# Performance work log

Hardware: AMD Instinct MI355X
Metric: run time of the kernel (lower is better)

Reference implementation:

```python
import jax, jax.numpy as jnp
import numpy as np

N = 100_000   # nodes
E = 1_600_000 # edges
V = 100_000   # vocab
G = 256       # graphs in batch
D = 64        # emb/hidden dim


def setup_inputs() -> dict:
    key = jax.random.key(0)
    ks = jax.random.split(key, 12)
    x_tokens = jax.random.randint(ks[0], (N, 1), 0, V)
    edge_index = jax.random.randint(ks[1], (2, E), 0, N)
    batch = jnp.sort(jax.random.randint(ks[2], (N,), 0, G))
    s = 0.02
    return {
        "x_tokens": x_tokens,
        "edge_index": edge_index,
        "batch": batch,
        "emb_table": jax.random.normal(ks[3], (V, D), jnp.float32) * s,
        "W0": jax.random.normal(ks[4], (D, D), jnp.float32) * s,
        "b0": jnp.zeros((D,), jnp.float32),
        "W1": jax.random.normal(ks[5], (D, D), jnp.float32) * s,
        "b1": jnp.zeros((D,), jnp.float32),
        "W2": jax.random.normal(ks[6], (D, D), jnp.float32) * s,
        "b2": jnp.zeros((D,), jnp.float32),
        "Wc1": jax.random.normal(ks[7], (2 * D, D), jnp.float32) * s,
        "bc1": jnp.zeros((D,), jnp.float32),
        "Wc2": jax.random.normal(ks[8], (D, 2), jnp.float32) * s,
        "bc2": jnp.zeros((2,), jnp.float32),
    }


def _gcn_norm(edge_index, n_nodes):
    # add self loops, compute symmetric normalization coefficients
    loop = jnp.arange(n_nodes, dtype=edge_index.dtype)
    src = jnp.concatenate([edge_index[0], loop])
    dst = jnp.concatenate([edge_index[1], loop])
    deg = jax.ops.segment_sum(jnp.ones_like(dst, jnp.float32), dst, num_segments=n_nodes)
    dinv = jnp.where(deg > 0, deg ** -0.5, 0.0)
    norm = dinv[src] * dinv[dst]  # [E+N]
    return src, dst, norm


def _gcn_conv(x, W, b, src, dst, norm, n_nodes):
    x = x @ W                                   # [N, D]
    msg = x[src] * norm[:, None]                # gather + scale, [E+N, D]
    out = jax.ops.segment_sum(msg, dst, num_segments=n_nodes)
    return out + b


def reference(x_tokens, edge_index, batch, emb_table, W0, b0, W1, b1, W2, b2, Wc1, bc1, Wc2, bc2):
    n = x_tokens.shape[0]
    src, dst, norm = _gcn_norm(edge_index, n)
    x = emb_table[x_tokens[:, 0]]               # [N, D]
    for W, b in ((W0, b0), (W1, b1), (W2, b2)):
        x = jax.nn.relu(_gcn_conv(x, W, b, src, dst, norm, n))
    # dual pooling over graph ids
    cnt = jax.ops.segment_sum(jnp.ones((n,), x.dtype), batch, num_segments=G)
    h_sum = jax.ops.segment_sum(x, batch, num_segments=G)
    h_mean = h_sum / jnp.maximum(cnt, 1.0)[:, None]
    h_max = jax.ops.segment_max(x, batch, num_segments=G)
    h_max = jnp.where(jnp.isfinite(h_max), h_max, 0.0)
    h = jnp.concatenate([h_mean, h_max], axis=-1)   # [G, 2D]
    logits = jax.nn.relu(h @ Wc1 + bc1) @ Wc2 + bc2  # [G, 2]
    return logits
```

## Files before the change

kernel.cpp:

```cpp
#include <hip/hip_runtime.h>
#include <hip/hip_fp16.h>
#include <math.h>


#define BKT_LOG 9
#define BKT (1 << BKT_LOG)
#define CHUNK 4096

typedef _Float16 h2 __attribute__((ext_vector_type(2)));
typedef _Float16 f16x8 __attribute__((ext_vector_type(8)));
typedef float f32x4 __attribute__((ext_vector_type(4)));

union HU { unsigned u; h2 h; };
__device__ inline h2 h2bits(unsigned u) { HU x; x.u = u; return x.h; }

#if __has_builtin(__builtin_amdgcn_fdot2)
#define FDOT2(a, b, c) __builtin_amdgcn_fdot2((a), (b), (c), false)
#else
__device__ inline float FDOT2(h2 a, h2 b, float c) {
  return (float)a.x * (float)b.x + (float)a.y * (float)b.y + c;
}
#endif

#define MASK_X 0x00003C00u
#define MASK_Y 0x3C000000u

__device__ inline void acc8c(const uint4& v, float* acc) {
  const unsigned* w = (const unsigned*)&v;
#pragma unroll
  for (int k = 0; k < 4; k++) {
    h2 hv = h2bits(w[k]);
    acc[2 * k]     = FDOT2(hv, h2bits(MASK_X), acc[2 * k]);
    acc[2 * k + 1] = FDOT2(hv, h2bits(MASK_Y), acc[2 * k + 1]);
  }
}

__global__ __launch_bounds__(256) void k_wcvt(const float* __restrict__ W0,
                                              const float* __restrict__ W1,
                                              const float* __restrict__ W2,
                                              _Float16* __restrict__ Wf,
                                              int* __restrict__ chist,
                                              float* __restrict__ hz, int hzn) {
  if (blockIdx.x < 3) {
    const float* W = (blockIdx.x == 0) ? W0 : (blockIdx.x == 1) ? W1 : W2;
    _Float16* out = Wf + blockIdx.x * 4096;
    for (int i = threadIdx.x; i < 4096; i += 256) {
      int c = i >> 10, s = (i >> 9) & 1, l = (i >> 3) & 63, j = i & 7;
      int k = 32 * s + 8 * (l >> 4) + j;
      int ncol = 16 * c + (l & 15);
      out[i] = (_Float16)W[k * 64 + ncol];
    }
  } else if (blockIdx.x == 3) {
    chist[threadIdx.x] = 0;
  } else {
    for (int i = threadIdx.x; i < hzn; i += 256) hz[i] = 0.f;
  }
}

__global__ __launch_bounds__(256) void k_chist(const int* __restrict__ dst,
                                               int* __restrict__ chist, int E, int B) {
  __shared__ int h[256];
  h[threadIdx.x] = 0;
  __syncthreads();
  for (long e = (long)blockIdx.x * blockDim.x + threadIdx.x; e < E;
       e += (long)gridDim.x * blockDim.x)
    atomicAdd(&h[dst[e] >> BKT_LOG], 1);
  __syncthreads();
  if (threadIdx.x < B && h[threadIdx.x]) atomicAdd(&chist[threadIdx.x], h[threadIdx.x]);
}

__global__ __launch_bounds__(256) void k_cscan(const int* __restrict__ chist,
                                               int* __restrict__ cbase,
                                               int* __restrict__ gcur, int E, int B) {
  __shared__ int s[256];
  int v = (threadIdx.x < B) ? chist[threadIdx.x] : 0;
  s[threadIdx.x] = v;
  __syncthreads();
  for (int d = 1; d < 256; d <<= 1) {
    int t = (threadIdx.x >= (unsigned)d) ? s[threadIdx.x - d] : 0;
    __syncthreads();
    s[threadIdx.x] += t;
    __syncthreads();
  }
  if (threadIdx.x < B) {
    int ex = s[threadIdx.x] - v;
    cbase[threadIdx.x] = ex;
    gcur[threadIdx.x] = ex;
  }
  if (threadIdx.x == B) cbase[B] = E;
}

__global__ __launch_bounds__(256) void k_part(const int* __restrict__ src,
                                              const int* __restrict__ dst,
                                              int* __restrict__ gcur,
                                              int* __restrict__ ebuf, int E, int B) {
  __shared__ int sA[CHUNK];
  __shared__ int dA[CHUNK];
  __shared__ int h[256], base[256];
  int tid = threadIdx.x;
  long c0 = (long)blockIdx.x * CHUNK;
  int m = (int)min((long)CHUNK, (long)E - c0);
  h[tid] = 0;
  __syncthreads();
  for (int i = tid; i < m; i += 256) {
    int s = src[c0 + i];
    int d = dst[c0 + i];
    sA[i] = s;
    dA[i] = d;
    atomicAdd(&h[d >> BKT_LOG], 1);
  }
  __syncthreads();
  if (tid < B && h[tid]) base[tid] = atomicAdd(&gcur[tid], h[tid]);
  __syncthreads();
  h[tid] = 0;
  __syncthreads();
  for (int i = tid; i < m; i += 256) {
    int s = sA[i], d = dA[i];
    int k = d >> BKT_LOG;
    int p = base[k] + atomicAdd(&h[k], 1);
    ebuf[p] = ((d & (BKT - 1)) << 17) | s;
  }
}

__global__ __launch_bounds__(512) void k_bplace(const int* __restrict__ ebuf,
                                                const int* __restrict__ cbase,
                                                int* __restrict__ off,
                                                int* __restrict__ csrc,
                                                float* __restrict__ dinv,
                                                int N, int E) {
  __shared__ int s[512];
  __shared__ int cur[512];
  int b = blockIdx.x, tid = threadIdx.x;
  int n0 = b << BKT_LOG;
  int nn = min(BKT, N - n0);
  int e0 = cbase[b], e1 = cbase[b + 1];
  s[tid] = 0;
  __syncthreads();
  for (int e = e0 + tid; e < e1; e += 512) atomicAdd(&s[ebuf[e] >> 17], 1);
  __syncthreads();
  int deg = s[tid];
  for (int d = 1; d < 512; d <<= 1) {
    int t = (tid >= d) ? s[tid - d] : 0;
    __syncthreads();
    s[tid] += t;
    __syncthreads();
  }
  int excl = s[tid] - deg;
  if (tid < nn) {
    off[n0 + tid] = e0 + excl;
    dinv[n0 + tid] = 1.0f / sqrtf((float)(1 + deg));
  }
  cur[tid] = excl;
  __syncthreads();
  for (int e = e0 + tid; e < e1; e += 512) {
    int p = ebuf[e];
    int pos = e0 + atomicAdd(&cur[p >> 17], 1);
    csrc[pos] = p & 0x1FFFF;
  }
  if (b == 0 && tid == 0) off[N] = E;
}

template <bool EMB>
__global__ __launch_bounds__(256) void k_mfmamm(const _Float16* __restrict__ y,
                                                const int* __restrict__ tok,
                                                const float* __restrict__ emb,
                                                const _Float16* __restrict__ Wf,
                                                const float* __restrict__ dinv,
                                                float scale,
                                                _Float16* __restrict__ xh,
                                                int n, int npad) {
  __shared__ _Float16 lds[4 * 16 * 72];
  int w = threadIdx.x >> 6, l = threadIdx.x & 63;
  int m = l & 15, q = l >> 4;
  int rbase = blockIdx.x * 64 + w * 16;

  f16x8 a0, a1;
  if (EMB) {
    int node = min(rbase + m, n - 1);
    const float* er = emb + (size_t)tok[node] * 64;
    float4 v0 = *(const float4*)(er + q * 8);
    float4 v1 = *(const float4*)(er + q * 8 + 4);
    float4 v2 = *(const float4*)(er + 32 + q * 8);
    float4 v3 = *(const float4*)(er + 32 + q * 8 + 4);
    a0[0] = (_Float16)v0.x; a0[1] = (_Float16)v0.y; a0[2] = (_Float16)v0.z; a0[3] = (_Float16)v0.w;
    a0[4] = (_Float16)v1.x; a0[5] = (_Float16)v1.y; a0[6] = (_Float16)v1.z; a0[7] = (_Float16)v1.w;
    a1[0] = (_Float16)v2.x; a1[1] = (_Float16)v2.y; a1[2] = (_Float16)v2.z; a1[3] = (_Float16)v2.w;
    a1[4] = (_Float16)v3.x; a1[5] = (_Float16)v3.y; a1[6] = (_Float16)v3.z; a1[7] = (_Float16)v3.w;
  } else {
    int node = rbase + m;
    a0 = *(const f16x8*)(y + ((size_t)(q >> 1) * npad + node) * 16 + (q & 1) * 8);
    a1 = *(const f16x8*)(y + ((size_t)((q >> 1) + 2) * npad + node) * 16 + (q & 1) * 8);
  }
  float4 d4 = *(const float4*)(dinv + rbase + q * 4);

  const f16x8* wf = (const f16x8*)Wf + l;
  f32x4 acc[4];
#pragma unroll
  for (int c = 0; c < 4; c++) {
    f32x4 z = {0.f, 0.f, 0.f, 0.f};
    z = __builtin_amdgcn_mfma_f32_16x16x32_f16(a0, wf[(c * 2 + 0) * 64], z, 0, 0, 0);
    z = __builtin_amdgcn_mfma_f32_16x16x32_f16(a1, wf[(c * 2 + 1) * 64], z, 0, 0, 0);
    acc[c] = z;
  }

  const float ds[4] = {d4.x * scale, d4.y * scale, d4.z * scale, d4.w * scale};
  _Float16* ldw = lds + w * 16 * 72;
#pragma unroll
  for (int c = 0; c < 4; c++)
#pragma unroll
    for (int r = 0; r < 4; r++)
      ldw[(q * 4 + r) * 72 + c * 16 + m] = (_Float16)(acc[c][r] * ds[r]);
  __syncthreads();

  int row2 = l & 15, c2 = l >> 4;
  int node = rbase + row2;
  if (node < n) {
    const uint4* s4 = (const uint4*)(ldw + row2 * 72 + c2 * 16);
    uint4 v0 = s4[0], v1 = s4[1];
    uint4* dst = (uint4*)(xh + ((size_t)c2 * npad + node) * 16);
    dst[0] = v0;
    dst[1] = v1;
  }
}

__global__ __launch_bounds__(256) void k_aggregate(const int* __restrict__ off,
                                                   const int* __restrict__ csrc,
                                                   const float* __restrict__ dinv,
                                                   const _Float16* __restrict__ xh,
                                                   const float* __restrict__ bias,
                                                   _Float16* __restrict__ outp,
                                                   int n, int npad) {
  int c = blockIdx.x & 3;
  int lane = threadIdx.x & 63;
  int n4 = lane >> 4, g = (lane >> 1) & 7, o = lane & 1;
  int t = (blockIdx.x >> 2) * 16 + (threadIdx.x >> 6) * 4 + n4;
  bool valid = t < n;
  int tc = valid ? t : n - 1;
  int e0 = off[tc], e1 = off[tc + 1];
  if (!valid) e1 = e0;
  const uint4* x4 = (const uint4*)xh + (size_t)c * npad * 2;

  float acc[8];
#pragma unroll
  for (int k = 0; k < 8; k++) acc[k] = 0.f;
  if (g == 0) acc8c(x4[(size_t)tc * 2 + o], acc);

  int it = e0 + g;
  int s = (it < e1) ? csrc[it] : 0;
  while (it < e1) {
    int itn = it + 8;
    int sn = (itn < e1) ? csrc[itn] : 0;
    uint4 v = x4[(size_t)s * 2 + o];
    acc8c(v, acc);
    s = sn;
    it = itn;
  }

#pragma unroll
  for (int mm = 2; mm <= 8; mm <<= 1) {
#pragma unroll
    for (int k = 0; k < 8; k++) acc[k] += __shfl_xor(acc[k], mm);
  }

  if (valid && g == 0) {
    float sc = dinv[t] * (1.0f / 256.0f);
    int f0 = c * 16 + o * 8;
    float4 bb0 = *(const float4*)(bias + f0);
    float4 bb1 = *(const float4*)(bias + f0 + 4);
    const float bs[8] = {bb0.x, bb0.y, bb0.z, bb0.w, bb1.x, bb1.y, bb1.z, bb1.w};
    _Float16 hh[8];
#pragma unroll
    for (int k = 0; k < 8; k++)
      hh[k] = (_Float16)(fmaxf(acc[k] * sc + bs[k], 0.f) * 4096.f);
    *(uint4*)(outp + ((size_t)c * npad + t) * 16 + o * 8) = *(const uint4*)hh;
  }
}

__global__ __launch_bounds__(256) void k_pool(const _Float16* __restrict__ x,
                                              const int* __restrict__ batch,
                                              float* __restrict__ hsum,
                                              float* __restrict__ hmax,
                                              int* __restrict__ cntg,
                                              int n, int npad) {
  int wid = (blockIdx.x * blockDim.x + threadIdx.x) >> 6;
  int lane = threadIdx.x & 63;
  int i0 = wid * 64;
  if (i0 >= n) return;
  int i1 = min(i0 + 64, n);
  size_t sb = (size_t)(lane >> 4) * npad * 16 + (lane & 15);
  int batch_l = (i0 + lane < n) ? batch[i0 + lane] : 0;
  float gsum = 0.f, gmax = 0.f;
  int cur = __shfl(batch_l, 0);
  int c = 0;
  for (int i = i0; i < i1; i++) {
    int g = __shfl(batch_l, i - i0);
    if (g != cur) {
      atomicAdd(&hsum[cur * 64 + lane], gsum);
      atomicMax((int*)&hmax[cur * 64 + lane], __float_as_int(gmax));
      if (lane == 0) atomicAdd(&cntg[cur], c);
      gsum = 0.f; gmax = 0.f; c = 0; cur = g;
    }
    float v = (float)x[sb + (size_t)i * 16];
    gsum += v;
    gmax = fmaxf(gmax, v);
    c++;
  }
  atomicAdd(&hsum[cur * 64 + lane], gsum);
  atomicMax((int*)&hmax[cur * 64 + lane], __float_as_int(gmax));
  if (lane == 0) atomicAdd(&cntg[cur], c);
}

__global__ __launch_bounds__(64) void k_cls(const float* __restrict__ hsum,
                                            const float* __restrict__ hmax,
                                            const int* __restrict__ cnt,
                                            const float* __restrict__ Wc1,
                                            const float* __restrict__ bc1,
                                            const float* __restrict__ Wc2,
                                            const float* __restrict__ bc2,
                                            float* __restrict__ out) {
  __shared__ float h[128];
  __shared__ float hid[64];
  int g = blockIdx.x, j = threadIdx.x;
  int c = cnt[g];
  float cf = (float)(c > 0 ? c : 1);
  h[j] = hsum[g * 64 + j] / cf * (1.0f / 4096.0f);
  h[64 + j] = hmax[g * 64 + j] * (1.0f / 4096.0f);
  __syncthreads();
  float acc = bc1[j];
  for (int k = 0; k < 128; k++) acc += h[k] * Wc1[k * 64 + j];
  hid[j] = fmaxf(acc, 0.f);
  __syncthreads();
  if (j < 2) {
    float a = bc2[j];
    for (int k = 0; k < 64; k++) a += hid[k] * Wc2[k * 2 + j];
    out[g * 2 + j] = a;
  }
}

extern "C" void kernel_launch(void* const* d_in, const int* in_sizes, int n_in,
                              void* d_out, int out_size, void* d_ws, size_t ws_size,
                              hipStream_t stream) {
  const int N = in_sizes[0];
  const int E = in_sizes[1] / 2;
  const int G = out_size / 2;
  const int B = (N + BKT - 1) >> BKT_LOG;
  const int Npad = (N + 63) & ~63;

  const int* tok   = (const int*)d_in[0];
  const int* ei    = (const int*)d_in[1];
  const int* batch = (const int*)d_in[2];
  const float* emb = (const float*)d_in[3];
  const float* W0 = (const float*)d_in[4];  const float* b0 = (const float*)d_in[5];
  const float* W1 = (const float*)d_in[6];  const float* b1 = (const float*)d_in[7];
  const float* W2 = (const float*)d_in[8];  const float* b2 = (const float*)d_in[9];
  const float* Wc1 = (const float*)d_in[10]; const float* bc1 = (const float*)d_in[11];
  const float* Wc2 = (const float*)d_in[12]; const float* bc2 = (const float*)d_in[13];
  const int* srcp = ei;
  const int* dstp = ei + E;

  int* off    = (int*)d_ws;
  int* csrc   = off + N + 2;
  float* dinv = (float*)(csrc + E);
  int* chist  = (int*)(dinv + Npad);
  int* cbase  = chist + 256;
  int* gcur   = cbase + 256;
  _Float16* Wf = (_Float16*)(gcur + 256);
  _Float16* xh = Wf + 3 * 4096;
  _Float16* y  = xh + (size_t)Npad * 64;
  int* ebuf   = (int*)(y + (size_t)Npad * 64);
  float* hsum = (float*)(ebuf + E);
  float* hmax = hsum + (size_t)G * 64;
  int*   cntg = (int*)(hmax + (size_t)G * 64);

  auto cdiv = [](long a, long b) { return (int)((a + b - 1) / b); };
  const int aggBlocks = 4 * cdiv(N, 16);

  k_wcvt<<<5, 256, 0, stream>>>(W0, W1, W2, Wf, chist, hsum, G * 129);

  k_chist<<<cdiv(E, CHUNK), 256, 0, stream>>>(dstp, chist, E, B);
  k_cscan<<<1, 256, 0, stream>>>(chist, cbase, gcur, E, B);
  k_part<<<cdiv(E, CHUNK), 256, 0, stream>>>(srcp, dstp, gcur, ebuf, E, B);
  k_bplace<<<B, 512, 0, stream>>>(ebuf, cbase, off, csrc, dinv, N, E);

  k_mfmamm<true><<<cdiv(N, 64), 256, 0, stream>>>(nullptr, tok, emb, Wf, dinv, 256.f, xh, N, Npad);
  k_aggregate<<<aggBlocks, 256, 0, stream>>>(off, csrc, dinv, xh, b0, y, N, Npad);

  k_mfmamm<false><<<cdiv(N, 64), 256, 0, stream>>>(y, nullptr, nullptr, Wf + 4096, dinv, 1.f / 16.f, xh, N, Npad);
  k_aggregate<<<aggBlocks, 256, 0, stream>>>(off, csrc, dinv, xh, b1, y, N, Npad);

  k_mfmamm<false><<<cdiv(N, 64), 256, 0, stream>>>(y, nullptr, nullptr, Wf + 8192, dinv, 1.f / 16.f, xh, N, Npad);
  k_aggregate<<<aggBlocks, 256, 0, stream>>>(off, csrc, dinv, xh, b2, y, N, Npad);

  k_pool<<<cdiv(N, 256), 256, 0, stream>>>(y, batch, hsum, hmax, cntg, N, Npad);

  k_cls<<<G, 64, 0, stream>>>(hsum, hmax, cntg, Wc1, bc1, Wc2, bc2, (float*)d_out);
}
```

Measured before the change: 371.8 us.

## Fold bucket scan into histogram via last-block pattern; unroll aggregate gather by two

Removes the separate single-block scan launch by having the last block of the histogram kernel (detected with an atomic counter and threadfence) perform the prefix scan. Separately, the aggregation edge loop now issues two neighbor row loads per iteration with index prefetch, raising memory-level parallelism. This saves one launch and gap at the cost of an extra counter reset and more registers in the aggregation kernel.

```diff
diff --git a/kernel.cpp b/kernel.cpp
--- a/kernel.cpp
+++ b/kernel.cpp
@@ -40,6 +40,7 @@
                                               const float* __restrict__ W2,
                                               _Float16* __restrict__ Wf,
                                               int* __restrict__ chist,
+                                              int* __restrict__ done,
                                               float* __restrict__ hz, int hzn) {
   if (blockIdx.x < 3) {
     const float* W = (blockIdx.x == 0) ? W0 : (blockIdx.x == 1) ? W1 : W2;
@@ -52,14 +53,20 @@
     }
   } else if (blockIdx.x == 3) {
     chist[threadIdx.x] = 0;
+    if (threadIdx.x == 0) *done = 0;
   } else {
     for (int i = threadIdx.x; i < hzn; i += 256) hz[i] = 0.f;
   }
 }
 
 __global__ __launch_bounds__(256) void k_chist(const int* __restrict__ dst,
-                                               int* __restrict__ chist, int E, int B) {
+                                               int* __restrict__ chist,
+                                               int* __restrict__ cbase,
+                                               int* __restrict__ gcur,
+                                               int* __restrict__ done,
+                                               int E, int B) {
   __shared__ int h[256];
+  __shared__ int last;
   h[threadIdx.x] = 0;
   __syncthreads();
   for (long e = (long)blockIdx.x * blockDim.x + threadIdx.x; e < E;
@@ -67,23 +74,21 @@
     atomicAdd(&h[dst[e] >> BKT_LOG], 1);
   __syncthreads();
   if (threadIdx.x < B && h[threadIdx.x]) atomicAdd(&chist[threadIdx.x], h[threadIdx.x]);
-}
-
-__global__ __launch_bounds__(256) void k_cscan(const int* __restrict__ chist,
-                                               int* __restrict__ cbase,
-                                               int* __restrict__ gcur, int E, int B) {
-  __shared__ int s[256];
-  int v = (threadIdx.x < B) ? chist[threadIdx.x] : 0;
-  s[threadIdx.x] = v;
+  __threadfence();
+  if (threadIdx.x == 0) last = (atomicAdd(done, 1) == (int)gridDim.x - 1);
+  __syncthreads();
+  if (!last) return;
+  int v = (threadIdx.x < B) ? atomicAdd(&chist[threadIdx.x], 0) : 0;
+  h[threadIdx.x] = v;
   __syncthreads();
   for (int d = 1; d < 256; d <<= 1) {
-    int t = (threadIdx.x >= (unsigned)d) ? s[threadIdx.x - d] : 0;
+    int t = (threadIdx.x >= (unsigned)d) ? h[threadIdx.x - d] : 0;
     __syncthreads();
-    s[threadIdx.x] += t;
+    h[threadIdx.x] += t;
     __syncthreads();
   }
   if (threadIdx.x < B) {
-    int ex = s[threadIdx.x] - v;
+    int ex = h[threadIdx.x] - v;
     cbase[threadIdx.x] = ex;
     gcur[threadIdx.x] = ex;
   }
@@ -245,15 +250,23 @@
   for (int k = 0; k < 8; k++) acc[k] = 0.f;
   if (g == 0) acc8c(x4[(size_t)tc * 2 + o], acc);
 
-  int it = e0 + g;
-  int s = (it < e1) ? csrc[it] : 0;
-  while (it < e1) {
-    int itn = it + 8;
-    int sn = (itn < e1) ? csrc[itn] : 0;
-    uint4 v = x4[(size_t)s * 2 + o];
-    acc8c(v, acc);
-    s = sn;
-    it = itn;
+  int iA = e0 + g;
+  bool aA = iA < e1, aB = iA + 8 < e1;
+  int sA = aA ? csrc[iA] : 0;
+  int sB = aB ? csrc[iA + 8] : 0;
+  while (aA) {
+    uint4 vA = x4[(size_t)sA * 2 + o];
+    uint4 vB;
+    if (aB) vB = x4[(size_t)sB * 2 + o];
+    int iN = iA + 16;
+    bool aN = iN < e1, aM = iN + 8 < e1;
+    int sN = 0, sM = 0;
+    if (aN) sN = csrc[iN];
+    if (aM) sM = csrc[iN + 8];
+    acc8c(vA, acc);
+    if (aB) acc8c(vB, acc);
+    iA = iN; aA = aN; sA = sN;
+    aB = aM; sB = sM;
   }
 
 #pragma unroll
@@ -364,7 +377,8 @@
   int* chist  = (int*)(dinv + Npad);
   int* cbase  = chist + 256;
   int* gcur   = cbase + 256;
-  _Float16* Wf = (_Float16*)(gcur + 256);
+  int* done   = gcur + 256;
+  _Float16* Wf = (_Float16*)(done + 2);
   _Float16* xh = Wf + 3 * 4096;
   _Float16* y  = xh + (size_t)Npad * 64;
   int* ebuf   = (int*)(y + (size_t)Npad * 64);
@@ -375,10 +389,9 @@
   auto cdiv = [](long a, long b) { return (int)((a + b - 1) / b); };
   const int aggBlocks = 4 * cdiv(N, 16);
 
-  k_wcvt<<<5, 256, 0, stream>>>(W0, W1, W2, Wf, chist, hsum, G * 129);
-
-  k_chist<<<cdiv(E, CHUNK), 256, 0, stream>>>(dstp, chist, E, B);
-  k_cscan<<<1, 256, 0, stream>>>(chist, cbase, gcur, E, B);
+  k_wcvt<<<5, 256, 0, stream>>>(W0, W1, W2, Wf, chist, done, hsum, G * 129);
+
+  k_chist<<<cdiv(E, CHUNK), 256, 0, stream>>>(dstp, chist, cbase, gcur, done, E, B);
   k_part<<<cdiv(E, CHUNK), 256, 0, stream>>>(srcp, dstp, gcur, ebuf, E, B);
   k_bplace<<<B, 512, 0, stream>>>(ebuf, cbase, off, csrc, dinv, N, E);
 
```

Result: slower. 382.2 us (+2.8%).

## Fuse graph pooling into final aggregate and double-issue edge gathers

Applied to the files above, without the earlier changes.

The last GCN aggregation now performs segment sum/max pooling directly from shared memory, removing the separate pool kernel and the write/read of the final fp16 activations. Pooling stays in fp32 without the 4096 fixed-point scale, so the classifier no longer rescales. The edge loop is also unrolled by two, so each lane issues two neighbour gathers per iteration for more memory-level parallelism. In exchange, the number of pooling atomics rises, since each block of 16 nodes issues its own atomics per graph segment.

```diff
diff --git a/kernel.cpp b/kernel.cpp
--- a/kernel.cpp
+++ b/kernel.cpp
@@ -223,17 +223,25 @@
   }
 }
 
+template <bool POOL>
 __global__ __launch_bounds__(256) void k_aggregate(const int* __restrict__ off,
                                                    const int* __restrict__ csrc,
                                                    const float* __restrict__ dinv,
                                                    const _Float16* __restrict__ xh,
                                                    const float* __restrict__ bias,
                                                    _Float16* __restrict__ outp,
+                                                   const int* __restrict__ batch,
+                                                   float* __restrict__ hsum,
+                                                   float* __restrict__ hmax,
+                                                   int* __restrict__ cntg,
                                                    int n, int npad) {
+  __shared__ float sm[16][17];
+  __shared__ int sb[16];
   int c = blockIdx.x & 3;
   int lane = threadIdx.x & 63;
   int n4 = lane >> 4, g = (lane >> 1) & 7, o = lane & 1;
-  int t = (blockIdx.x >> 2) * 16 + (threadIdx.x >> 6) * 4 + n4;
+  int tbase = (blockIdx.x >> 2) * 16;
+  int t = tbase + (threadIdx.x >> 6) * 4 + n4;
   bool valid = t < n;
   int tc = valid ? t : n - 1;
   int e0 = off[tc], e1 = off[tc + 1];
@@ -245,15 +253,23 @@
   for (int k = 0; k < 8; k++) acc[k] = 0.f;
   if (g == 0) acc8c(x4[(size_t)tc * 2 + o], acc);
 
-  int it = e0 + g;
-  int s = (it < e1) ? csrc[it] : 0;
-  while (it < e1) {
-    int itn = it + 8;
-    int sn = (itn < e1) ? csrc[itn] : 0;
-    uint4 v = x4[(size_t)s * 2 + o];
-    acc8c(v, acc);
-    s = sn;
-    it = itn;
+  int iA = e0 + g;
+  bool aA = iA < e1, aB = iA + 8 < e1;
+  int sA = aA ? csrc[iA] : 0;
+  int sB = aB ? csrc[iA + 8] : 0;
+  while (aA) {
+    uint4 vA = x4[(size_t)sA * 2 + o];
+    uint4 vB;
+    if (aB) vB = x4[(size_t)sB * 2 + o];
+    int iN = iA + 16;
+    bool aN = iN < e1, aM = iN + 8 < e1;
+    int sN = 0, sM = 0;
+    if (aN) sN = csrc[iN];
+    if (aM) sM = csrc[iN + 8];
+    acc8c(vA, acc);
+    if (aB) acc8c(vB, acc);
+    iA = iN; aA = aN; sA = sN;
+    aB = aM; sB = sM;
   }
 
 #pragma unroll
@@ -262,52 +278,62 @@
     for (int k = 0; k < 8; k++) acc[k] += __shfl_xor(acc[k], mm);
   }
 
-  if (valid && g == 0) {
-    float sc = dinv[t] * (1.0f / 256.0f);
-    int f0 = c * 16 + o * 8;
-    float4 bb0 = *(const float4*)(bias + f0);
-    float4 bb1 = *(const float4*)(bias + f0 + 4);
-    const float bs[8] = {bb0.x, bb0.y, bb0.z, bb0.w, bb1.x, bb1.y, bb1.z, bb1.w};
-    _Float16 hh[8];
-#pragma unroll
-    for (int k = 0; k < 8; k++)
-      hh[k] = (_Float16)(fmaxf(acc[k] * sc + bs[k], 0.f) * 4096.f);
-    *(uint4*)(outp + ((size_t)c * npad + t) * 16 + o * 8) = *(const uint4*)hh;
-  }
-}
-
-__global__ __launch_bounds__(256) void k_pool(const _Float16* __restrict__ x,
-                                              const int* __restrict__ batch,
-                                              float* __restrict__ hsum,
-                                              float* __restrict__ hmax,
-                                              int* __restrict__ cntg,
-                                              int n, int npad) {
-  int wid = (blockIdx.x * blockDim.x + threadIdx.x) >> 6;
-  int lane = threadIdx.x & 63;
-  int i0 = wid * 64;
-  if (i0 >= n) return;
-  int i1 = min(i0 + 64, n);
-  size_t sb = (size_t)(lane >> 4) * npad * 16 + (lane & 15);
-  int batch_l = (i0 + lane < n) ? batch[i0 + lane] : 0;
-  float gsum = 0.f, gmax = 0.f;
-  int cur = __shfl(batch_l, 0);
-  int c = 0;
-  for (int i = i0; i < i1; i++) {
-    int g = __shfl(batch_l, i - i0);
-    if (g != cur) {
-      atomicAdd(&hsum[cur * 64 + lane], gsum);
-      atomicMax((int*)&hmax[cur * 64 + lane], __float_as_int(gmax));
-      if (lane == 0) atomicAdd(&cntg[cur], c);
-      gsum = 0.f; gmax = 0.f; c = 0; cur = g;
+  if (POOL) {
+    int ni = (threadIdx.x >> 6) * 4 + n4;
+    if (valid && g == 0) {
+      float sc = dinv[t] * (1.0f / 256.0f);
+      int f0 = c * 16 + o * 8;
+      float4 bb0 = *(const float4*)(bias + f0);
+      float4 bb1 = *(const float4*)(bias + f0 + 4);
+      const float bs[8] = {bb0.x, bb0.y, bb0.z, bb0.w, bb1.x, bb1.y, bb1.z, bb1.w};
+#pragma unroll
+      for (int k = 0; k < 8; k++)
+        sm[ni][o * 8 + k] = fmaxf(acc[k] * sc + bs[k], 0.f);
     }
-    float v = (float)x[sb + (size_t)i * 16];
-    gsum += v;
-    gmax = fmaxf(gmax, v);
-    c++;
-  }
-  atomicAdd(&hsum[cur * 64 + lane], gsum);
-  atomicMax((int*)&hmax[cur * 64 + lane], __float_as_int(gmax));
-  if (lane == 0) atomicAdd(&cntg[cur], c);
+    if (threadIdx.x < 16) {
+      int tt = tbase + threadIdx.x;
+      sb[threadIdx.x] = (tt < n) ? batch[tt] : -1;
+    }
+    __syncthreads();
+    if (threadIdx.x < 16) {
+      int f = threadIdx.x;
+      int fg = c * 16 + f;
+      float rs = 0.f, rm = 0.f;
+      int curb = sb[0], run = 0;
+      for (int i = 0; i < 16; i++) {
+        int bi = sb[i];
+        if (bi < 0) break;
+        if (bi != curb) {
+          atomicAdd(&hsum[curb * 64 + fg], rs);
+          atomicMax((int*)&hmax[curb * 64 + fg], __float_as_int(rm));
+          if (f == 0 && c == 0) atomicAdd(&cntg[curb], run);
+          rs = 0.f; rm = 0.f; run = 0; curb = bi;
+        }
+        float v = sm[i][f];
+        rs += v;
+        rm = fmaxf(rm, v);
+        run++;
+      }
+      if (run > 0 && curb >= 0) {
+        atomicAdd(&hsum[curb * 64 + fg], rs);
+        atomicMax((int*)&hmax[curb * 64 + fg], __float_as_int(rm));
+        if (f == 0 && c == 0) atomicAdd(&cntg[curb], run);
+      }
+    }
+  } else {
+    if (valid && g == 0) {
+      float sc = dinv[t] * (1.0f / 256.0f);
+      int f0 = c * 16 + o * 8;
+      float4 bb0 = *(const float4*)(bias + f0);
+      float4 bb1 = *(const float4*)(bias + f0 + 4);
+      const float bs[8] = {bb0.x, bb0.y, bb0.z, bb0.w, bb1.x, bb1.y, bb1.z, bb1.w};
+      _Float16 hh[8];
+#pragma unroll
+      for (int k = 0; k < 8; k++)
+        hh[k] = (_Float16)(fmaxf(acc[k] * sc + bs[k], 0.f) * 4096.f);
+      *(uint4*)(outp + ((size_t)c * npad + t) * 16 + o * 8) = *(const uint4*)hh;
+    }
+  }
 }
 
 __global__ __launch_bounds__(64) void k_cls(const float* __restrict__ hsum,
@@ -323,8 +349,8 @@
   int g = blockIdx.x, j = threadIdx.x;
   int c = cnt[g];
   float cf = (float)(c > 0 ? c : 1);
-  h[j] = hsum[g * 64 + j] / cf * (1.0f / 4096.0f);
-  h[64 + j] = hmax[g * 64 + j] * (1.0f / 4096.0f);
+  h[j] = hsum[g * 64 + j] / cf;
+  h[64 + j] = hmax[g * 64 + j];
   __syncthreads();
   float acc = bc1[j];
   for (int k = 0; k < 128; k++) acc += h[k] * Wc1[k * 64 + j];
@@ -383,15 +409,16 @@
   k_bplace<<<B, 512, 0, stream>>>(ebuf, cbase, off, csrc, dinv, N, E);
 
   k_mfmamm<true><<<cdiv(N, 64), 256, 0, stream>>>(nullptr, tok, emb, Wf, dinv, 256.f, xh, N, Npad);
-  k_aggregate<<<aggBlocks, 256, 0, stream>>>(off, csrc, dinv, xh, b0, y, N, Npad);
+  k_aggregate<false><<<aggBlocks, 256, 0, stream>>>(off, csrc, dinv, xh, b0, y,
+                                                    nullptr, nullptr, nullptr, nullptr, N, Npad);
 
   k_mfmamm<false><<<cdiv(N, 64), 256, 0, stream>>>(y, nullptr, nullptr, Wf + 4096, dinv, 1.f / 16.f, xh, N, Npad);
-  k_aggregate<<<aggBlocks, 256, 0, stream>>>(off, csrc, dinv, xh, b1, y, N, Npad);
+  k_aggregate<false><<<aggBlocks, 256, 0, stream>>>(off, csrc, dinv, xh, b1, y,
+                                                    nullptr, nullptr, nullptr, nullptr, N, Npad);
 
   k_mfmamm<false><<<cdiv(N, 64), 256, 0, stream>>>(y, nullptr, nullptr, Wf + 8192, dinv, 1.f / 16.f, xh, N, Npad);
-  k_aggregate<<<aggBlocks, 256, 0, stream>>>(off, csrc, dinv, xh, b2, y, N, Npad);
-
-  k_pool<<<cdiv(N, 256), 256, 0, stream>>>(y, batch, hsum, hmax, cntg, N, Npad);
+  k_aggregate<true><<<aggBlocks, 256, 0, stream>>>(off, csrc, dinv, xh, b2, nullptr,
+                                                   batch, hsum, hmax, cntg, N, Npad);
 
   k_cls<<<G, 64, 0, stream>>>(hsum, hmax, cntg, Wc1, bc1, Wc2, bc2, (float*)d_out);
 }
```

Result: no change. 367.6 us (-1.1%).
